# Kernel tuning notes

Measured on AMD Instinct MI355X. Metric: run time of the kernel, lower is better.

Reference implementation:

```python
import jax, jax.numpy as jnp
import numpy as np

B, S, H, D = 2, 4096, 16, 128  # batch, seq, heads, head_dim
HID = H * D                    # 2048 hidden size
C = 128                        # chunk size for the chunked recurrent scan
EPS = 1e-6


def setup_inputs() -> dict:
    key = jax.random.key(0)
    ks = jax.random.split(key, 9)
    sc = 0.02  # initializer_range
    w = lambda k: jax.random.normal(k, (HID, HID), jnp.float32) * sc
    return {
        "x": jax.random.normal(ks[0], (B, S, HID), jnp.float32),
        "Wq": w(ks[1]), "bq": jnp.zeros((HID,), jnp.float32),
        "Wk": w(ks[2]), "bk": jnp.zeros((HID,), jnp.float32),
        "Wv": w(ks[3]), "bv": jnp.zeros((HID,), jnp.float32),
        "Wo": w(ks[4]), "bo": jnp.zeros((HID,), jnp.float32),
    }


def reference(x, Wq, bq, Wk, bk, Wv, bv, Wo, bo):
    Bx, Sx, hid = x.shape
    NC = Sx // C  # number of chunks

    q = (x @ Wq + bq).reshape(Bx, Sx, H, D)
    k = (x @ Wk + bk).reshape(Bx, Sx, H, D)
    v = (x @ Wv + bv).reshape(Bx, Sx, H, D)

    # positive feature map for linear attention
    qf = jax.nn.elu(q) + 1.0
    kf = jax.nn.elu(k) + 1.0

    # chunk: [B, NC, C, H, D]
    qf = qf.reshape(Bx, NC, C, H, D)
    kf = kf.reshape(Bx, NC, C, H, D)
    vc = v.reshape(Bx, NC, C, H, D)

    # inter-chunk recurrent state: exclusive cumulative sums of per-chunk KV outer
    kv = jnp.einsum('bnchd,bnche->bnhde', kf, vc)      # per-chunk KV state
    kv_ex = jnp.cumsum(kv, axis=1) - kv                # exclusive prefix state
    ksum = kf.sum(axis=2)                              # [B,NC,H,D]
    ksum_ex = jnp.cumsum(ksum, axis=1) - ksum          # exclusive normalizer state

    inter = jnp.einsum('bnchd,bnhde->bnche', qf, kv_ex)
    z_inter = jnp.einsum('bnchd,bnhd->bnch', qf, ksum_ex)

    # intra-chunk causal attention (masked matmul)
    A = jnp.einsum('bnchd,bnkhd->bnhck', qf, kf)       # [B,NC,H,C,C]
    causal = jnp.tril(jnp.ones((C, C), dtype=bool))
    A = jnp.where(causal[None, None, None], A, 0.0)
    intra = jnp.einsum('bnhck,bnkhe->bnche', A, vc)
    z_intra = jnp.swapaxes(A.sum(-1), 2, 3)            # [B,NC,C,H]

    out = (inter + intra) / (z_inter + z_intra + EPS)[..., None]
    out = out.reshape(Bx, Sx, hid)
    return out @ Wo + bo
```

## Files before the change

kernel.cpp:

```cpp
#include <hip/hip_runtime.h>

typedef unsigned short u16;
typedef unsigned int u32;
typedef unsigned long long u64;
typedef __attribute__((ext_vector_type(8))) short short8;
typedef __attribute__((ext_vector_type(4))) float f32x4;
typedef __attribute__((ext_vector_type(4))) int int4v;

constexpr int Bsz = 2, Ssz = 4096, Hn = 16, Dh = 128, HID = 2048;
constexpr int Cch = 128, NCh = 32;
constexpr float EPSf = 1e-6f;

#define MFMA16 __builtin_amdgcn_mfma_f32_16x16x32_bf16
#define VMW(N) asm volatile("s_waitcnt vmcnt(" #N ")" ::: "memory")

__device__ __forceinline__ float b2f(u16 u) {
  unsigned int i = ((unsigned int)u) << 16;
  return __builtin_bit_cast(float, i);
}
__device__ __forceinline__ u16 f2b(float f) {
  unsigned int i = __builtin_bit_cast(unsigned int, f);
  i += 0x7fffu + ((i >> 16) & 1u);
  return (u16)(i >> 16);
}

__device__ __forceinline__ void gload_lds16(const u16* g, u16* l) {
  __builtin_amdgcn_global_load_lds(
      (const __attribute__((address_space(1))) u32*)g,
      (__attribute__((address_space(3))) u32*)l, 16, 0, 0);
}

__global__ __launch_bounds__(256) void cvt_bf16(const float* __restrict__ x,
                                                u16* __restrict__ xb)
{
  const size_t n8 = (size_t)Bsz * Ssz * HID / 8;
  for (size_t i = (size_t)blockIdx.x * 256 + threadIdx.x; i < n8;
       i += (size_t)gridDim.x * 256) {
    const f32x4 a = *(const f32x4*)&x[i * 8];
    const f32x4 b = *(const f32x4*)&x[i * 8 + 4];
    u16 tmp[8];
#pragma unroll
    for (int u = 0; u < 4; ++u) { tmp[u] = f2b(a[u]); tmp[u + 4] = f2b(b[u]); }
    *(int4v*)&xb[i * 8] = *(const int4v*)tmp;
  }
}

__global__ __launch_bounds__(256) void transpose4(
    const float* __restrict__ A0, const float* __restrict__ A1,
    const float* __restrict__ A2, const float* __restrict__ A3,
    u16* __restrict__ T0, u16* __restrict__ T1,
    u16* __restrict__ T2, u16* __restrict__ T3)
{
  constexpr int N = HID, LDT = 72;
  const int z = blockIdx.z;
  const float* __restrict__ A = (z == 0) ? A0 : (z == 1) ? A1 : (z == 2) ? A2 : A3;
  u16* __restrict__ T = (z == 0) ? T0 : (z == 1) ? T1 : (z == 2) ? T2 : T3;
  __shared__ u16 lds[64 * LDT];
  const int t = threadIdx.x;
  const int i = t >> 3, j = (t & 7) * 8;
  const int r0 = blockIdx.y * 64, c0 = blockIdx.x * 64;
#pragma unroll
  for (int half = 0; half < 2; ++half) {
    const int r = i + half * 32;
    const f32x4 a = *(const f32x4*)&A[(size_t)(r0 + r) * N + c0 + j];
    const f32x4 b = *(const f32x4*)&A[(size_t)(r0 + r) * N + c0 + j + 4];
    u16 tmp[8];
#pragma unroll
    for (int u = 0; u < 4; ++u) { tmp[u] = f2b(a[u]); tmp[u + 4] = f2b(b[u]); }
    *(int4v*)&lds[r * LDT + j] = *(const int4v*)tmp;
  }
  __syncthreads();
#pragma unroll
  for (int half = 0; half < 2; ++half) {
    const int c = i + half * 32;
    u16 tmp[8];
#pragma unroll
    for (int u = 0; u < 8; ++u) tmp[u] = lds[(j + u) * LDT + c];
    *(int4v*)&T[(size_t)(c0 + c) * N + r0 + j] = *(const int4v*)tmp;
  }
}

template <int OUTF32>
__global__ __launch_bounds__(512) void gemm2blk(
    const u16* __restrict__ A,
    const u16* __restrict__ W0T, const u16* __restrict__ W1T, const u16* __restrict__ W2T,
    const float* __restrict__ bb0, const float* __restrict__ bb1, const float* __restrict__ bb2,
    void* __restrict__ o0, void* __restrict__ o1, void* __restrict__ o2,
    int elu_mask)
{
  constexpr int K = HID, N = HID;
  extern __shared__ u16 lds[];

  const int z = blockIdx.z;
  const u16* __restrict__ WT    = (z == 0) ? W0T : (z == 1) ? W1T : W2T;
  const float* __restrict__ bias = (z == 0) ? bb0 : (z == 1) ? bb1 : bb2;
  void* __restrict__ outv = (z == 0) ? o0 : (z == 1) ? o1 : o2;
  const bool elu = (elu_mask >> z) & 1;

  const int lid = blockIdx.x + 8 * blockIdx.y;
  const int k8 = lid & 7, j32 = lid >> 3;
  const int m0 = (k8 * 4 + (j32 >> 3)) * 256;
  const int n0 = (j32 & 7) * 256;

  const int t = threadIdx.x, lane = t & 63, w = t >> 6;
  const int wm = w >> 2, wn = w & 3;
  const int l15 = lane & 15, lg = lane >> 4;
  const int sl2 = (l15 >> 1) & 3;

  const int strow = lane >> 2;
  const int stslot = (lane & 3) ^ ((lane >> 3) & 3);
  const u16* gA = A  + (size_t)(m0 + w * 16 + strow) * K + stslot * 8;
  const u16* gB = WT + (size_t)(n0 + w * 16 + strow) * K + stslot * 8;

  const int aRow = (wm * 128 + l15) * 32 + ((lg ^ sl2) << 3);
  const int bRow = 8192 + (wn * 64 + l15) * 32 + ((lg ^ sl2) << 3);
  u16* const lw = &lds[w * 512];

  f32x4 acc[8][4] = {};
  short8 aF[8], bF[4];

#define STAGE4(SB) do {                                                       \
    gload_lds16(gA,                   lw + (SB)*16384);                       \
    gload_lds16(gA + (size_t)128*K,   lw + (SB)*16384 + 4096);                \
    gload_lds16(gB,                   lw + (SB)*16384 + 8192);                \
    gload_lds16(gB + (size_t)128*K,   lw + (SB)*16384 + 8192 + 4096);         \
    gA += 32; gB += 32;                                                       \
  } while (0)

#define WINDOW(BUF, PF) do {                                                  \
    VMW(0);                                                                   \
    __builtin_amdgcn_s_barrier();                                             \
    if (PF) STAGE4((BUF)^1);                                                  \
    _Pragma("unroll")                                                         \
    for (int i = 0; i < 8; ++i)                                               \
      aF[i] = *(const short8*)&lds[(BUF)*16384 + aRow + i*512];               \
    _Pragma("unroll")                                                         \
    for (int j = 0; j < 4; ++j)                                               \
      bF[j] = *(const short8*)&lds[(BUF)*16384 + bRow + j*512];               \
    __builtin_amdgcn_s_setprio(1);                                            \
    _Pragma("unroll")                                                         \
    for (int i = 0; i < 8; ++i) {                                             \
      acc[i][0] = MFMA16(aF[i], bF[0], acc[i][0], 0, 0, 0);                   \
      acc[i][1] = MFMA16(aF[i], bF[1], acc[i][1], 0, 0, 0);                   \
      acc[i][2] = MFMA16(aF[i], bF[2], acc[i][2], 0, 0, 0);                   \
      acc[i][3] = MFMA16(aF[i], bF[3], acc[i][3], 0, 0, 0);                   \
    }                                                                         \
    __builtin_amdgcn_s_setprio(0);                                            \
  } while (0)

  STAGE4(0);

  for (int W = 0; W < 64; W += 2) {
    WINDOW(0, (W + 1) < 64);
    WINDOW(1, (W + 2) < 64);
  }

#pragma unroll
  for (int j = 0; j < 4; ++j) {
    const int col = n0 + wn * 64 + j * 16 + l15;
    const float bv = bias[col];
#pragma unroll
    for (int i = 0; i < 8; ++i) {
      const int row0 = m0 + wm * 128 + i * 16 + lg * 4;
#pragma unroll
      for (int r = 0; r < 4; ++r) {
        float v = acc[i][j][r] + bv;
        if (elu) v = (v > 0.0f) ? (v + 1.0f) : __expf(v);
        if (OUTF32) ((float*)outv)[(size_t)(row0 + r) * N + col] = v;
        else        ((u16*)outv)[(size_t)(row0 + r) * N + col] = f2b(v);
      }
    }
  }
#undef STAGE4
#undef WINDOW
}

__global__ __launch_bounds__(256) void pass1_kv(
    const u16* __restrict__ KF, const u16* __restrict__ V,
    u16* __restrict__ KVT, float* __restrict__ KSUM)
{
  constexpr int LD = 136;
  __shared__ u16 lk[128 * LD];
  __shared__ u16 lv[128 * LD];
  __shared__ float kp[256];
  const int bnh = blockIdx.x;
  const int h = bnh % Hn, n = (bnh / Hn) % NCh, b = bnh / (Hn * NCh);
  const size_t rowbase = (size_t)(b * Ssz + n * Cch) * HID + h * Dh;
  const int t = threadIdx.x, lane = t & 63, w = t >> 6;
  const int wr = (w >> 1) * 64, wc = (w & 1) * 64;
  const int l15 = lane & 15, lg = lane >> 4;
  const int sr = t >> 4, sc = (t & 15) * 8;

#pragma unroll
  for (int rep = 0; rep < 8; ++rep) {
    const int r = rep * 16 + sr;
    *(int4v*)&lk[r * LD + sc] = *(const int4v*)&KF[rowbase + (size_t)r * HID + sc];
    *(int4v*)&lv[r * LD + sc] = *(const int4v*)&V[rowbase + (size_t)r * HID + sc];
  }
  __syncthreads();

  {
    const int col = t & 127, hf = t >> 7;
    float s = 0.0f;
    for (int c = hf * 64; c < hf * 64 + 64; ++c) s += b2f(lk[c * LD + col]);
    kp[t] = s;
  }
  __syncthreads();
  if (t < 128) KSUM[(size_t)bnh * Dh + t] = kp[t] + kp[t + 128];

  f32x4 acc[4][4] = {};
#pragma unroll
  for (int kk = 0; kk < 4; ++kk) {
    const int cb = kk * 32 + lg * 8;
    short8 aF[4], bF[4];
#pragma unroll
    for (int i = 0; i < 4; ++i) {
      const int e = wr + i * 16 + l15;
      short8 a;
#pragma unroll
      for (int u = 0; u < 8; ++u) a[u] = (short)lv[(cb + u) * LD + e];
      aF[i] = a;
    }
#pragma unroll
    for (int j = 0; j < 4; ++j) {
      const int d = wc + j * 16 + l15;
      short8 bb;
#pragma unroll
      for (int u = 0; u < 8; ++u) bb[u] = (short)lk[(cb + u) * LD + d];
      bF[j] = bb;
    }
#pragma unroll
    for (int i = 0; i < 4; ++i)
#pragma unroll
      for (int j = 0; j < 4; ++j)
        acc[i][j] = MFMA16(aF[i], bF[j], acc[i][j], 0, 0, 0);
  }

  u16* __restrict__ outp = KVT + (size_t)bnh * (Dh * Dh);
#pragma unroll
  for (int i = 0; i < 4; ++i) {
    const int e0 = wr + i * 16 + lg * 4;
#pragma unroll
    for (int j = 0; j < 4; ++j) {
      const int d = wc + j * 16 + l15;
#pragma unroll
      for (int r = 0; r < 4; ++r)
        outp[(size_t)(e0 + r) * Dh + d] = f2b(acc[i][j][r]);
    }
  }
}

__global__ __launch_bounds__(256) void cumsum_all(u16* __restrict__ KVT,
                                                  float* __restrict__ KS)
{
  const int nkv = (Bsz * Hn * Dh * Dh) / 256;
  if ((int)blockIdx.x < nkv) {
    const int tid = blockIdx.x * 256 + threadIdx.x;
    const int ed = tid & (Dh * Dh - 1);
    const int bh = tid >> 14;
    const int h = bh % Hn, b = bh / Hn;
    const size_t base = ((size_t)(b * NCh * Hn) + h) * (Dh * Dh) + ed;
    const size_t stride = (size_t)Hn * Dh * Dh;
    float s = 0.0f;
    for (int n = 0; n < NCh; ++n) {
      const size_t idx = base + (size_t)n * stride;
      const float v = b2f(KVT[idx]);
      KVT[idx] = f2b(s);
      s += v;
    }
  } else {
    const int tid = (blockIdx.x - nkv) * 256 + threadIdx.x;
    const int d = tid & (Dh - 1);
    const int bh = tid >> 7;
    const int h = bh % Hn, b = bh / Hn;
    const size_t base = ((size_t)(b * NCh * Hn) + h) * Dh + d;
    const size_t stride = (size_t)Hn * Dh;
    float s = 0.0f;
    for (int n = 0; n < NCh; ++n) {
      const size_t idx = base + (size_t)n * stride;
      const float v = KS[idx];
      KS[idx] = s;
      s += v;
    }
  }
}

__global__ __launch_bounds__(256) void pass2_attn(
    const u16* __restrict__ QF, const u16* __restrict__ KF, const u16* __restrict__ V,
    const u16* __restrict__ KVT, const float* __restrict__ KSE,
    u16* __restrict__ Y)
{
  constexpr int LD = 136;
  __shared__ u16 smem[4 * 128 * LD];
  __shared__ float zpart[2][128];
  u16* sQ  = smem;
  u16* sK  = smem + 128 * LD;
  u16* sA  = smem + 2 * 128 * LD;
  u16* sKV = smem + 3 * 128 * LD;

  const int bnh = blockIdx.x;
  const int h = bnh % Hn, n = (bnh / Hn) % NCh, b = bnh / (Hn * NCh);
  const size_t rowbase = (size_t)(b * Ssz + n * Cch) * HID + h * Dh;
  const int t = threadIdx.x, lane = t & 63, w = t >> 6;
  const int wr = (w >> 1) * 64, wc = (w & 1) * 64;
  const int l15 = lane & 15, lg = lane >> 4;
  const int sr = t >> 4, sc = (t & 15) * 8;

  const u16* __restrict__ kvsrc = KVT + (size_t)bnh * (Dh * Dh);
#pragma unroll
  for (int rep = 0; rep < 8; ++rep) {
    const int r = rep * 16 + sr;
    *(int4v*)&sQ[r * LD + sc]  = *(const int4v*)&QF[rowbase + (size_t)r * HID + sc];
    *(int4v*)&sK[r * LD + sc]  = *(const int4v*)&KF[rowbase + (size_t)r * HID + sc];
    *(int4v*)&sKV[r * LD + sc] = *(const int4v*)&kvsrc[r * Dh + sc];
  }
  __syncthreads();

  f32x4 acc[4][4] = {};
#pragma unroll
  for (int kk = 0; kk < 4; ++kk) {
    const int krd = kk * 32 + lg * 8;
    short8 aF[4], bF[4];
#pragma unroll
    for (int i = 0; i < 4; ++i)
      aF[i] = *(const short8*)&sQ[(wr + i * 16 + l15) * LD + krd];
#pragma unroll
    for (int j = 0; j < 4; ++j)
      bF[j] = *(const short8*)&sK[(wc + j * 16 + l15) * LD + krd];
#pragma unroll
    for (int i = 0; i < 4; ++i)
#pragma unroll
      for (int j = 0; j < 4; ++j)
        acc[i][j] = MFMA16(aF[i], bF[j], acc[i][j], 0, 0, 0);
  }
#pragma unroll
  for (int i = 0; i < 4; ++i) {
    const int c0 = wr + i * 16 + lg * 4;
#pragma unroll
    for (int j = 0; j < 4; ++j) {
      const int ck = wc + j * 16 + l15;
#pragma unroll
      for (int r = 0; r < 4; ++r) {
        const int c = c0 + r;
        sA[c * LD + ck] = f2b((ck <= c) ? acc[i][j][r] : 0.0f);
      }
    }
  }
  __syncthreads();

  if (t < 128) {
    const float* kse = KSE + (size_t)bnh * Dh;
    float zz = 0.0f;
    for (int d2 = 0; d2 < 128; ++d2) zz += b2f(sQ[t * LD + d2]) * kse[d2];
    zpart[0][t] = zz;
  } else {
    const int row = t - 128;
    float zz = 0.0f;
    for (int ck = 0; ck < 128; ++ck) zz += b2f(sA[row * LD + ck]);
    zpart[1][row] = zz;
  }
#pragma unroll
  for (int rep = 0; rep < 8; ++rep) {
    const int r = rep * 16 + sr;
    *(int4v*)&sK[r * LD + sc] = *(const int4v*)&V[rowbase + (size_t)r * HID + sc];
  }
  __syncthreads();

  f32x4 o[4][4] = {};
#pragma unroll
  for (int kk = 0; kk < 4; ++kk) {
    const int krd = kk * 32 + lg * 8;
    short8 aF[4], bF[4];
#pragma unroll
    for (int i = 0; i < 4; ++i)
      aF[i] = *(const short8*)&sA[(wr + i * 16 + l15) * LD + krd];
#pragma unroll
    for (int j = 0; j < 4; ++j) {
      const int e = wc + j * 16 + l15;
      short8 bb;
#pragma unroll
      for (int u = 0; u < 8; ++u) bb[u] = (short)sK[(krd + u) * LD + e];
      bF[j] = bb;
    }
#pragma unroll
    for (int i = 0; i < 4; ++i)
#pragma unroll
      for (int j = 0; j < 4; ++j)
        o[i][j] = MFMA16(aF[i], bF[j], o[i][j], 0, 0, 0);
  }
#pragma unroll
  for (int kk = 0; kk < 4; ++kk) {
    const int krd = kk * 32 + lg * 8;
    short8 aF[4], bF[4];
#pragma unroll
    for (int i = 0; i < 4; ++i)
      aF[i] = *(const short8*)&sQ[(wr + i * 16 + l15) * LD + krd];
#pragma unroll
    for (int j = 0; j < 4; ++j)
      bF[j] = *(const short8*)&sKV[(wc + j * 16 + l15) * LD + krd];
#pragma unroll
    for (int i = 0; i < 4; ++i)
#pragma unroll
      for (int j = 0; j < 4; ++j)
        o[i][j] = MFMA16(aF[i], bF[j], o[i][j], 0, 0, 0);
  }

#pragma unroll
  for (int i = 0; i < 4; ++i) {
    const int c0 = wr + i * 16 + lg * 4;
#pragma unroll
    for (int j = 0; j < 4; ++j) {
      const int e = wc + j * 16 + l15;
#pragma unroll
      for (int r = 0; r < 4; ++r) {
        const int c = c0 + r;
        const float zz = zpart[0][c] + zpart[1][c] + EPSf;
        Y[rowbase + (size_t)c * HID + e] = f2b(o[i][j][r] / zz);
      }
    }
  }
}

extern "C" void kernel_launch(void* const* d_in, const int* in_sizes, int n_in,
                              void* d_out, int out_size, void* d_ws, size_t ws_size,
                              hipStream_t stream)
{
  const float* x  = (const float*)d_in[0];
  const float* Wq = (const float*)d_in[1];
  const float* bq = (const float*)d_in[2];
  const float* Wk = (const float*)d_in[3];
  const float* bk = (const float*)d_in[4];
  const float* Wv = (const float*)d_in[5];
  const float* bv = (const float*)d_in[6];
  const float* Wo = (const float*)d_in[7];
  const float* bo = (const float*)d_in[8];
  float* out = (float*)d_out;

  char* p = (char*)d_ws;
  auto take = [&](size_t bytes) { char* q = p; p += (bytes + 255) & ~(size_t)255; return q; };
  u16* WqT = (u16*)take((size_t)HID * HID * 2);
  u16* WkT = (u16*)take((size_t)HID * HID * 2);
  u16* WvT = (u16*)take((size_t)HID * HID * 2);
  u16* WoT = (u16*)take((size_t)HID * HID * 2);
  u16* QF  = (u16*)take((size_t)Bsz * Ssz * HID * 2);
  u16* KFb = (u16*)take((size_t)Bsz * Ssz * HID * 2);
  u16* Vb  = (u16*)take((size_t)Bsz * Ssz * HID * 2);
  char* region = take((size_t)Bsz * Ssz * HID * 2);
  u16* xb  = (u16*)region;
  u16* KVT = (u16*)region;
  float* KS = (float*)take((size_t)Bsz * NCh * Hn * Dh * 4);
  u16* Yb = QF;

  (void)hipFuncSetAttribute((const void*)gemm2blk<0>,
                            hipFuncAttributeMaxDynamicSharedMemorySize, 65536);
  (void)hipFuncSetAttribute((const void*)gemm2blk<1>,
                            hipFuncAttributeMaxDynamicSharedMemorySize, 65536);

  dim3 blk(256, 1, 1);
  cvt_bf16<<<dim3(2048), blk, 0, stream>>>(x, xb);
  transpose4<<<dim3(HID / 64, HID / 64, 4), blk, 0, stream>>>(
      Wq, Wk, Wv, Wo, WqT, WkT, WvT, WoT);
  gemm2blk<0><<<dim3(HID / 256, (Bsz * Ssz) / 256, 3), dim3(512), 65536, stream>>>(
      xb, WqT, WkT, WvT, bq, bk, bv, QF, KFb, Vb, 0x3);
  pass1_kv<<<dim3(Bsz * NCh * Hn), blk, 0, stream>>>(KFb, Vb, KVT, KS);
  cumsum_all<<<dim3((Bsz * Hn * Dh * Dh) / 256 + (Bsz * Hn * Dh) / 256), blk, 0, stream>>>(KVT, KS);
  pass2_attn<<<dim3(Bsz * NCh * Hn), blk, 0, stream>>>(QF, KFb, Vb, KVT, KS, Yb);
  gemm2blk<1><<<dim3(HID / 256, (Bsz * Ssz) / 256, 1), dim3(512), 65536, stream>>>(
      Yb, WoT, WoT, WoT, bo, bo, bo, out, out, out, 0);
}
```

Before: 405.6 us.

## Deepen GEMM LDS pipeline to four stages with split-phase loads and MFMAs

Replaces the double-buffered GEMM main loop with a four-buffer pipeline that keeps three K-tiles in flight. Each K-step is split into two phases: the A and B prefetch issue is interleaved with half of the MFMAs, and the waits use partial vmcnt counts instead of draining all loads. The goal is to hide global-to-LDS latency behind more compute. In exchange it doubles dynamic LDS to 128 KB per block, which may limit occupancy, and adds extra barriers per step.

```diff
diff --git a/kernel.cpp b/kernel.cpp
--- a/kernel.cpp
+++ b/kernel.cpp
@@ -13,6 +13,7 @@
 
 #define MFMA16 __builtin_amdgcn_mfma_f32_16x16x32_bf16
 #define VMW(N) asm volatile("s_waitcnt vmcnt(" #N ")" ::: "memory")
+#define LGKM0  asm volatile("s_waitcnt lgkmcnt(0)" ::: "memory")
 
 __device__ __forceinline__ float b2f(u16 u) {
   unsigned int i = ((unsigned int)u) << 16;
@@ -81,7 +82,7 @@
 }
 
 template <int OUTF32>
-__global__ __launch_bounds__(512) void gemm2blk(
+__global__ __launch_bounds__(512) void gemm_fp(
     const u16* __restrict__ A,
     const u16* __restrict__ W0T, const u16* __restrict__ W1T, const u16* __restrict__ W2T,
     const float* __restrict__ bb0, const float* __restrict__ bb1, const float* __restrict__ bb2,
@@ -119,41 +120,71 @@
   f32x4 acc[8][4] = {};
   short8 aF[8], bF[4];
 
-#define STAGE4(SB) do {                                                       \
-    gload_lds16(gA,                   lw + (SB)*16384);                       \
-    gload_lds16(gA + (size_t)128*K,   lw + (SB)*16384 + 4096);                \
-    gload_lds16(gB,                   lw + (SB)*16384 + 8192);                \
-    gload_lds16(gB + (size_t)128*K,   lw + (SB)*16384 + 8192 + 4096);         \
-    gA += 32; gB += 32;                                                       \
-  } while (0)
-
-#define WINDOW(BUF, PF) do {                                                  \
-    VMW(0);                                                                   \
-    __builtin_amdgcn_s_barrier();                                             \
-    if (PF) STAGE4((BUF)^1);                                                  \
+#define PH1(BUF, SB, PF) do {                                                 \
     _Pragma("unroll")                                                         \
     for (int i = 0; i < 8; ++i)                                               \
       aF[i] = *(const short8*)&lds[(BUF)*16384 + aRow + i*512];               \
-    _Pragma("unroll")                                                         \
-    for (int j = 0; j < 4; ++j)                                               \
-      bF[j] = *(const short8*)&lds[(BUF)*16384 + bRow + j*512];               \
+    bF[0] = *(const short8*)&lds[(BUF)*16384 + bRow];                         \
+    bF[1] = *(const short8*)&lds[(BUF)*16384 + bRow + 512];                   \
+    if (PF) {                                                                 \
+      gload_lds16(gA,                 lw + (SB)*16384);                       \
+      gload_lds16(gA + (size_t)128*K, lw + (SB)*16384 + 4096);                \
+      gA += 32;                                                               \
+    }                                                                         \
+    __builtin_amdgcn_s_barrier();                                             \
+    LGKM0;                                                                    \
     __builtin_amdgcn_s_setprio(1);                                            \
     _Pragma("unroll")                                                         \
     for (int i = 0; i < 8; ++i) {                                             \
       acc[i][0] = MFMA16(aF[i], bF[0], acc[i][0], 0, 0, 0);                   \
       acc[i][1] = MFMA16(aF[i], bF[1], acc[i][1], 0, 0, 0);                   \
+    }                                                                         \
+    __builtin_amdgcn_s_setprio(0);                                            \
+    __builtin_amdgcn_s_barrier();                                             \
+  } while (0)
+
+#define PH2(BUF, SB, PF, VMN) do {                                            \
+    bF[2] = *(const short8*)&lds[(BUF)*16384 + bRow + 1024];                  \
+    bF[3] = *(const short8*)&lds[(BUF)*16384 + bRow + 1536];                  \
+    if (PF) {                                                                 \
+      gload_lds16(gB,                 lw + (SB)*16384 + 8192);                 \
+      gload_lds16(gB + (size_t)128*K, lw + (SB)*16384 + 8192 + 4096);          \
+      gB += 32;                                                               \
+    }                                                                         \
+    VMW(VMN);                                                                 \
+    __builtin_amdgcn_s_barrier();                                             \
+    LGKM0;                                                                    \
+    __builtin_amdgcn_s_setprio(1);                                            \
+    _Pragma("unroll")                                                         \
+    for (int i = 0; i < 8; ++i) {                                             \
       acc[i][2] = MFMA16(aF[i], bF[2], acc[i][2], 0, 0, 0);                   \
       acc[i][3] = MFMA16(aF[i], bF[3], acc[i][3], 0, 0, 0);                   \
     }                                                                         \
     __builtin_amdgcn_s_setprio(0);                                            \
+    __builtin_amdgcn_s_barrier();                                             \
   } while (0)
 
-  STAGE4(0);
-
-  for (int W = 0; W < 64; W += 2) {
-    WINDOW(0, (W + 1) < 64);
-    WINDOW(1, (W + 2) < 64);
-  }
+#pragma unroll
+  for (int pt = 0; pt < 3; ++pt) {
+    gload_lds16(gA,                 lw + pt*16384);
+    gload_lds16(gA + (size_t)128*K, lw + pt*16384 + 4096);
+    gload_lds16(gB,                 lw + pt*16384 + 8192);
+    gload_lds16(gB + (size_t)128*K, lw + pt*16384 + 8192 + 4096);
+    gA += 32; gB += 32;
+  }
+  VMW(8);
+  __builtin_amdgcn_s_barrier();
+
+  for (int W = 0; W < 60; W += 4) {
+    PH1(0, 3, 1); PH2(0, 3, 1, 8);
+    PH1(1, 0, 1); PH2(1, 0, 1, 8);
+    PH1(2, 1, 1); PH2(2, 1, 1, 8);
+    PH1(3, 2, 1); PH2(3, 2, 1, 8);
+  }
+  PH1(0, 3, 1); PH2(0, 3, 1, 8);
+  PH1(1, 0, 0); PH2(1, 0, 0, 4);
+  PH1(2, 0, 0); PH2(2, 0, 0, 0);
+  PH1(3, 0, 0); PH2(3, 0, 0, 0);
 
 #pragma unroll
   for (int j = 0; j < 4; ++j) {
@@ -171,8 +202,8 @@
       }
     }
   }
-#undef STAGE4
-#undef WINDOW
+#undef PH1
+#undef PH2
 }
 
 __global__ __launch_bounds__(256) void pass1_kv(
@@ -451,20 +482,20 @@
   float* KS = (float*)take((size_t)Bsz * NCh * Hn * Dh * 4);
   u16* Yb = QF;
 
-  (void)hipFuncSetAttribute((const void*)gemm2blk<0>,
-                            hipFuncAttributeMaxDynamicSharedMemorySize, 65536);
-  (void)hipFuncSetAttribute((const void*)gemm2blk<1>,
-                            hipFuncAttributeMaxDynamicSharedMemorySize, 65536);
+  (void)hipFuncSetAttribute((const void*)gemm_fp<0>,
+                            hipFuncAttributeMaxDynamicSharedMemorySize, 131072);
+  (void)hipFuncSetAttribute((const void*)gemm_fp<1>,
+                            hipFuncAttributeMaxDynamicSharedMemorySize, 131072);
 
   dim3 blk(256, 1, 1);
   cvt_bf16<<<dim3(2048), blk, 0, stream>>>(x, xb);
   transpose4<<<dim3(HID / 64, HID / 64, 4), blk, 0, stream>>>(
       Wq, Wk, Wv, Wo, WqT, WkT, WvT, WoT);
-  gemm2blk<0><<<dim3(HID / 256, (Bsz * Ssz) / 256, 3), dim3(512), 65536, stream>>>(
+  gemm_fp<0><<<dim3(HID / 256, (Bsz * Ssz) / 256, 3), dim3(512), 131072, stream>>>(
       xb, WqT, WkT, WvT, bq, bk, bv, QF, KFb, Vb, 0x3);
   pass1_kv<<<dim3(Bsz * NCh * Hn), blk, 0, stream>>>(KFb, Vb, KVT, KS);
   cumsum_all<<<dim3((Bsz * Hn * Dh * Dh) / 256 + (Bsz * Hn * Dh) / 256), blk, 0, stream>>>(KVT, KS);
   pass2_attn<<<dim3(Bsz * NCh * Hn), blk, 0, stream>>>(QF, KFb, Vb, KVT, KS, Yb);
-  gemm2blk<1><<<dim3(HID / 256, (Bsz * Ssz) / 256, 1), dim3(512), 65536, stream>>>(
+  gemm_fp<1><<<dim3(HID / 256, (Bsz * Ssz) / 256, 1), dim3(512), 131072, stream>>>(
       Yb, WoT, WoT, WoT, bo, bo, bo, out, out, out, 0);
 }
```

New measurement: 400.2 us. About the same (-1.3%).
